# Kernel optimization log

Hardware: AMD Instinct MI355X
Metric: run time of the kernel (lower is better)

The kernel has to match this reference:

```python
import jax, jax.numpy as jnp
import numpy as np

LATENT = 256
HIDDEN = 512
NODE_F = 128
MAX_NODES = 50
B = 128


def _mk_linear(key, fan_in, fan_out):
    kw, kb = jax.random.split(key)
    bound = 1.0 / np.sqrt(fan_in)
    W = jax.random.uniform(kw, (fan_in, fan_out), jnp.float32, -bound, bound)
    b = jax.random.uniform(kb, (fan_out,), jnp.float32, -bound, bound)
    return W, b


def setup_inputs() -> dict:
    key = jax.random.key(0)
    ks = jax.random.split(key, 7)
    z = jax.random.normal(ks[0], (B, LATENT), jnp.float32)
    # node decoder: latent -> hidden -> hidden -> max_nodes*node_features
    nw1, nb1 = _mk_linear(ks[1], LATENT, HIDDEN)
    nw2, nb2 = _mk_linear(ks[2], HIDDEN, HIDDEN)
    nw3, nb3 = _mk_linear(ks[3], HIDDEN, MAX_NODES * NODE_F)
    # edge decoder: latent + 2*node_features -> hidden -> hidden//2 -> 1
    ew1, eb1 = _mk_linear(ks[4], LATENT + 2 * NODE_F, HIDDEN)
    ew2, eb2 = _mk_linear(ks[5], HIDDEN, HIDDEN // 2)
    ew3, eb3 = _mk_linear(ks[6], HIDDEN // 2, 1)
    return {"z": z,
            "nw1": nw1, "nb1": nb1, "nw2": nw2, "nb2": nb2, "nw3": nw3, "nb3": nb3,
            "ew1": ew1, "eb1": eb1, "ew2": ew2, "eb2": eb2, "ew3": ew3, "eb3": eb3}


def reference(z, nw1, nb1, nw2, nb2, nw3, nb3, ew1, eb1, ew2, eb2, ew3, eb3):
    # ---- node decoder ----
    h = jax.nn.relu(z @ nw1 + nb1)
    h = jax.nn.relu(h @ nw2 + nb2)
    node_logits = h @ nw3 + nb3                      # [B, MAX_NODES*NODE_F]
    node_feats = node_logits.reshape(z.shape[0], MAX_NODES, NODE_F)
    node_probs = jax.nn.sigmoid(node_feats)

    # ---- edge decoder: vectorize the O(N^2) python loop over upper-tri pairs ----
    # jnp.triu_indices matches the torch loop order: i ascending, j ascending per i.
    ii, jj = jnp.triu_indices(MAX_NODES, k=1)        # [P] each, P = 1225
    ni = node_feats[:, ii, :]                        # [B, P, NODE_F]
    nj = node_feats[:, jj, :]                        # [B, P, NODE_F]
    zb = jnp.broadcast_to(z[:, None, :], (z.shape[0], ii.shape[0], z.shape[1]))
    edge_in = jnp.concatenate([zb, ni, nj], axis=-1)  # [B, P, LATENT+2*NODE_F]
    e = jax.nn.relu(edge_in @ ew1 + eb1)             # [B, P, HIDDEN]
    e = jax.nn.relu(e @ ew2 + eb2)                   # [B, P, HIDDEN//2]
    edge_probs = jax.nn.sigmoid(e @ ew3 + eb3)[..., 0]  # [B, P]
    return node_probs, edge_probs
```

## Files before the change

kernel.cpp:

```cpp
#include <hip/hip_runtime.h>
#include <math.h>

#define LATENT 256
#define HIDDEN 512
#define NODE_F 128
#define MAX_NODES 50
#define NPAIRS 1225
#define BATCH 128
#define NODE_OUT 6400
#define MTILE 64
#define PTILES 20

typedef __attribute__((ext_vector_type(8))) short short8;
typedef __attribute__((ext_vector_type(4))) float float4v;

__device__ __forceinline__ float bf2f(ushort u) {
    union { unsigned int i; float f; } v; v.i = ((unsigned int)u) << 16; return v.f;
}
__device__ __forceinline__ ushort f2bf(float f) {
    union { unsigned int i; float f; } v; v.f = f;
    unsigned int r = v.i + 0x7fffu + ((v.i >> 16) & 1u);
    return (ushort)(r >> 16);
}
__device__ __forceinline__ float sigmoidf(float x) {
    return 1.0f / (1.0f + __expf(-x));
}

#define TR3_B0   0
#define PREP_B0  800
#define ZC_B0    1824
#define ND_B0    2080
#define PT_B0    2336
#define PREPK_NB 2341

__global__ __launch_bounds__(256) void k_prep_all(
    const float* __restrict__ nw3, ushort* __restrict__ nw3T,
    const float* __restrict__ ew1, const float* __restrict__ ew2,
    ushort* __restrict__ ew2T, ushort* __restrict__ wijT,
    const float* __restrict__ z, const float* __restrict__ eb1,
    float* __restrict__ Zc,
    const float* __restrict__ nw1, const float* __restrict__ nb1,
    const float* __restrict__ nw2, const float* __restrict__ nb2,
    ushort* __restrict__ h2b, int* __restrict__ ptab)
{
    __shared__ float smem[64 * 65];
    int b = blockIdx.x;
    int tid = threadIdx.x;

    if (b < PREP_B0) {
        int bb = b - TR3_B0;
        int k0 = (bb & 7) * 64;
        int n0 = (bb >> 3) * 64;
        int tx = tid & 63, ty = tid >> 6;
#pragma unroll
        for (int r = 0; r < 16; r++) {
            int row = r * 4 + ty;
            smem[row * 65 + tx] = nw3[(k0 + row) * NODE_OUT + n0 + tx];
        }
        __syncthreads();
#pragma unroll
        for (int c = 0; c < 16; c++) {
            int n = c * 4 + ty;
            nw3T[(size_t)(n0 + n) * HIDDEN + k0 + tx] = f2bf(smem[tx * 65 + n]);
        }
    } else if (b < ZC_B0) {
        int t = (b - PREP_B0) * 256 + tid;
        if (t < 256 * 512) {
            int n = t >> 9, k = t & 511;
            ew2T[t] = f2bf(ew2[k * 256 + n]);
        } else {
            int u = t - 256 * 512;
            int n = u >> 7, k = u & 127;
            float s = (n < 512) ? ew1[(256 + k) * 512 + n] : ew1[(384 + k) * 512 + (n - 512)];
            wijT[u] = f2bf(s);
        }
    } else if (b < ND_B0) {
        int b2 = b - ZC_B0;
        int r = b2 >> 1, o = (b2 & 1) * 256 + tid;
        float* zs = smem;
        zs[tid] = z[r * LATENT + tid];
        __syncthreads();
        float acc = 0.f;
#pragma unroll 8
        for (int k = 0; k < LATENT; k++) acc += zs[k] * ew1[k * HIDDEN + o];
        Zc[r * HIDDEN + o] = acc + eb1[o];
    } else if (b < PT_B0) {
        int b2 = b - ND_B0;
        int r = b2 >> 1, half = b2 & 1;
        float* zs = smem;
        float* hs = smem + 256;
        zs[tid] = z[r * LATENT + tid];
        __syncthreads();
        float a0 = 0.f, a1 = 0.f;
#pragma unroll 8
        for (int k = 0; k < LATENT; k++) {
            float zk = zs[k];
            a0 += zk * nw1[k * HIDDEN + tid];
            a1 += zk * nw1[k * HIDDEN + tid + 256];
        }
        hs[tid]       = fmaxf(a0 + nb1[tid], 0.f);
        hs[tid + 256] = fmaxf(a1 + nb1[tid + 256], 0.f);
        __syncthreads();
        int o = half * 256 + tid;
        float acc = 0.f;
#pragma unroll 8
        for (int k = 0; k < HIDDEN; k++) acc += hs[k] * nw2[k * HIDDEN + o];
        acc += nb2[o];
        h2b[r * HIDDEN + o] = f2bf(fmaxf(acc, 0.f));
    } else {
        int p = (b - PT_B0) * 256 + tid;
        if (p < NPAIRS) {
            int i = 0, off = 0;
            while (p - off >= MAX_NODES - 1 - i) { off += MAX_NODES - 1 - i; ++i; }
            int j = i + 1 + (p - off);
            ptab[p] = (i << 8) | j;
        }
    }
}

__global__ __launch_bounds__(256, 4) void k_node_out_mfma(
    const ushort* __restrict__ h2b, const ushort* __restrict__ nw3T,
    const float* __restrict__ nb3, float* __restrict__ node_probs,
    ushort* __restrict__ node_feats)
{
    int tid = threadIdx.x;
    int wave = tid >> 6, lane = tid & 63;
    int m16 = lane & 15, quad = lane >> 4;
    int n0 = (blockIdx.x >> 2) * 64;
    int m0 = (blockIdx.x & 3) * 32;
    int col = n0 + wave * 16 + m16;

    float4v acc[2];
    acc[0] = (float4v)(0.f); acc[1] = (float4v)(0.f);

    const ushort* bb = nw3T + (size_t)col * HIDDEN;
    const ushort* a0p = h2b + (m0 + m16) * HIDDEN;
    const ushort* a1p = h2b + (m0 + 16 + m16) * HIDDEN;
#pragma unroll
    for (int it = 0; it < 16; ++it) {
        int kk = it * 32 + quad * 8;
        short8 b = *(const short8*)(bb + kk);
        short8 a0 = *(const short8*)(a0p + kk);
        short8 a1 = *(const short8*)(a1p + kk);
        acc[0] = __builtin_amdgcn_mfma_f32_16x16x32_bf16(a0, b, acc[0], 0, 0, 0);
        acc[1] = __builtin_amdgcn_mfma_f32_16x16x32_bf16(a1, b, acc[1], 0, 0, 0);
    }
    float bias = nb3[col];
#pragma unroll
    for (int mt = 0; mt < 2; mt++)
#pragma unroll
        for (int t = 0; t < 4; t++) {
            int row = m0 + mt * 16 + quad * 4 + t;
            float v = acc[mt][t] + bias;
            node_probs[(size_t)row * NODE_OUT + col] = sigmoidf(v);
            node_feats[(size_t)row * NODE_OUT + col] = f2bf(v);
        }
}

__global__ __launch_bounds__(256, 4) void k_uv(
    const ushort* __restrict__ nf, const ushort* __restrict__ wijT,
    ushort* __restrict__ UV)
{
    int tid = threadIdx.x;
    int wave = tid >> 6, lane = tid & 63;
    int m16 = lane & 15, quad = lane >> 4;
    int bm = blockIdx.x >> 2, bn = blockIdx.x & 3;
    int base = bn * 256 + wave * 64;
    int r0 = bm * 64;

    float4v acc[4][4];
#pragma unroll
    for (int mt = 0; mt < 4; mt++)
#pragma unroll
        for (int nt = 0; nt < 4; nt++) acc[mt][nt] = (float4v)(0.f);

#pragma unroll
    for (int k0 = 0; k0 < NODE_F; k0 += 32) {
        int kk = k0 + quad * 8;
        short8 a0 = *(const short8*)(nf + (r0 + m16) * NODE_F + kk);
        short8 a1 = *(const short8*)(nf + (r0 + 16 + m16) * NODE_F + kk);
        short8 a2 = *(const short8*)(nf + (r0 + 32 + m16) * NODE_F + kk);
        short8 a3 = *(const short8*)(nf + (r0 + 48 + m16) * NODE_F + kk);
#pragma unroll
        for (int nt = 0; nt < 4; nt++) {
            int n = base + nt * 16 + m16;
            short8 b = *(const short8*)(wijT + n * NODE_F + kk);
            acc[0][nt] = __builtin_amdgcn_mfma_f32_16x16x32_bf16(a0, b, acc[0][nt], 0, 0, 0);
            acc[1][nt] = __builtin_amdgcn_mfma_f32_16x16x32_bf16(a1, b, acc[1][nt], 0, 0, 0);
            acc[2][nt] = __builtin_amdgcn_mfma_f32_16x16x32_bf16(a2, b, acc[2][nt], 0, 0, 0);
            acc[3][nt] = __builtin_amdgcn_mfma_f32_16x16x32_bf16(a3, b, acc[3][nt], 0, 0, 0);
        }
    }
#pragma unroll
    for (int nt = 0; nt < 4; nt++) {
        int colg = base + nt * 16 + m16;
#pragma unroll
        for (int mt = 0; mt < 4; mt++)
#pragma unroll
            for (int t = 0; t < 4; t++) {
                int rr = r0 + mt * 16 + quad * 4 + t;
                UV[(size_t)rr * 1024 + colg] = f2bf(acc[mt][nt][t]);
            }
    }
}

__global__ __launch_bounds__(512, 4) void k_edge6(
    const float* __restrict__ Zc, const ushort* __restrict__ UV,
    const ushort* __restrict__ ew2T, const float* __restrict__ ew3,
    const float* __restrict__ eb2, const float* __restrict__ eb3,
    const int* __restrict__ ptab, float* __restrict__ out_edges)
{
    __shared__ __align__(16) ushort h1[MTILE][HIDDEN + 8];
    __shared__ float part[MTILE][8];
    __shared__ int uo[MTILE], vo[MTILE];

    int blk = blockIdx.x;
    int b   = blk / PTILES;
    int t0  = (blk - b * PTILES) * MTILE;

    int tid = threadIdx.x;
    if (tid < MTILE) {
        int p = t0 + tid;
        if (p >= NPAIRS) p = NPAIRS - 1;
        int ij = ptab[p];
        uo[tid] = (b * MAX_NODES + (ij >> 8)) * 1024;
        vo[tid] = (b * MAX_NODES + (ij & 255)) * 1024 + 512;
    }

    int wave = tid >> 6, lane = tid & 63;
    int c8 = lane * 8;
    float4v zA = *(const float4v*)(Zc + b * HIDDEN + c8);
    float4v zB = *(const float4v*)(Zc + b * HIDDEN + c8 + 4);
    __syncthreads();

    short8 uu[8], vv[8];
#pragma unroll
    for (int rr = 0; rr < 8; rr++) {
        int r = wave * 8 + rr;
        uu[rr] = *(const short8*)(UV + uo[r] + c8);
        vv[rr] = *(const short8*)(UV + vo[r] + c8);
    }
#pragma unroll
    for (int rr = 0; rr < 8; rr++) {
        int r = wave * 8 + rr;
        short8 hh;
#pragma unroll
        for (int e = 0; e < 8; e++) {
            float zz = (e < 4) ? zA[e] : zB[e - 4];
            hh[e] = (short)f2bf(fmaxf(zz + bf2f((ushort)uu[rr][e]) + bf2f((ushort)vv[rr][e]), 0.f));
        }
        *(short8*)&h1[r][c8] = hh;
    }
    __syncthreads();

    int m16 = lane & 15, quad = lane >> 4;

    float eb2v[2], ew3v[2];
    const ushort* bbase[2];
#pragma unroll
    for (int nt = 0; nt < 2; nt++) {
        int col = wave * 32 + nt * 16 + m16;
        eb2v[nt] = eb2[col];
        ew3v[nt] = ew3[col];
        bbase[nt] = ew2T + col * HIDDEN;
    }

    float4v acc2[4][2];
#pragma unroll
    for (int mt = 0; mt < 4; mt++)
#pragma unroll
        for (int nt = 0; nt < 2; nt++) acc2[mt][nt] = (float4v)(0.f);

    int kk0 = quad * 8;
    short8 bp[2][2][2];
#pragma unroll
    for (int i = 0; i < 2; i++) {
        bp[0][i][0] = *(const short8*)(bbase[0] + i * 32 + kk0);
        bp[0][i][1] = *(const short8*)(bbase[1] + i * 32 + kk0);
    }
#pragma unroll
    for (int g = 0; g < 8; g++) {
        int cur = g & 1, nxt = cur ^ 1;
        if (g < 7) {
#pragma unroll
            for (int i = 0; i < 2; i++) {
                int kk = (g + 1) * 64 + i * 32 + kk0;
                bp[nxt][i][0] = *(const short8*)(bbase[0] + kk);
                bp[nxt][i][1] = *(const short8*)(bbase[1] + kk);
            }
        }
#pragma unroll
        for (int i = 0; i < 2; i++) {
            int kk = g * 64 + i * 32 + kk0;
            short8 a0 = *(const short8*)&h1[m16][kk];
            short8 a1 = *(const short8*)&h1[16 + m16][kk];
            short8 a2 = *(const short8*)&h1[32 + m16][kk];
            short8 a3 = *(const short8*)&h1[48 + m16][kk];
            acc2[0][0] = __builtin_amdgcn_mfma_f32_16x16x32_bf16(a0, bp[cur][i][0], acc2[0][0], 0, 0, 0);
            acc2[1][0] = __builtin_amdgcn_mfma_f32_16x16x32_bf16(a1, bp[cur][i][0], acc2[1][0], 0, 0, 0);
            acc2[2][0] = __builtin_amdgcn_mfma_f32_16x16x32_bf16(a2, bp[cur][i][0], acc2[2][0], 0, 0, 0);
            acc2[3][0] = __builtin_amdgcn_mfma_f32_16x16x32_bf16(a3, bp[cur][i][0], acc2[3][0], 0, 0, 0);
            acc2[0][1] = __builtin_amdgcn_mfma_f32_16x16x32_bf16(a0, bp[cur][i][1], acc2[0][1], 0, 0, 0);
            acc2[1][1] = __builtin_amdgcn_mfma_f32_16x16x32_bf16(a1, bp[cur][i][1], acc2[1][1], 0, 0, 0);
            acc2[2][1] = __builtin_amdgcn_mfma_f32_16x16x32_bf16(a2, bp[cur][i][1], acc2[2][1], 0, 0, 0);
            acc2[3][1] = __builtin_amdgcn_mfma_f32_16x16x32_bf16(a3, bp[cur][i][1], acc2[3][1], 0, 0, 0);
        }
    }

#pragma unroll
    for (int mt = 0; mt < 4; mt++)
#pragma unroll
        for (int t = 0; t < 4; t++) {
            float s = 0.f;
#pragma unroll
            for (int nt = 0; nt < 2; nt++)
                s += fmaxf(acc2[mt][nt][t] + eb2v[nt], 0.f) * ew3v[nt];
            s += __shfl_xor(s, 1);
            s += __shfl_xor(s, 2);
            s += __shfl_xor(s, 4);
            s += __shfl_xor(s, 8);
            if (m16 == 0) part[mt * 16 + quad * 4 + t][wave] = s;
        }
    __syncthreads();

    if (tid < MTILE && t0 + tid < NPAIRS) {
        float v = eb3[0];
#pragma unroll
        for (int w = 0; w < 8; w++) v += part[tid][w];
        out_edges[b * NPAIRS + t0 + tid] = sigmoidf(v);
    }
}

extern "C" void kernel_launch(void* const* d_in, const int* in_sizes, int n_in,
                              void* d_out, int out_size, void* d_ws, size_t ws_size,
                              hipStream_t stream) {
    const float* z   = (const float*)d_in[0];
    const float* nw1 = (const float*)d_in[1];
    const float* nb1 = (const float*)d_in[2];
    const float* nw2 = (const float*)d_in[3];
    const float* nb2 = (const float*)d_in[4];
    const float* nw3 = (const float*)d_in[5];
    const float* nb3 = (const float*)d_in[6];
    const float* ew1 = (const float*)d_in[7];
    const float* eb1 = (const float*)d_in[8];
    const float* ew2 = (const float*)d_in[9];
    const float* eb2 = (const float*)d_in[10];
    const float* ew3 = (const float*)d_in[11];
    const float* eb3 = (const float*)d_in[12];

    char* ws = (char*)d_ws;
    int*    ptab = (int*)(ws);
    ushort* h2b  = (ushort*)(ws + 262144);
    ushort* nf   = (ushort*)(ws + 393216);
    ushort* ew2T = (ushort*)(ws + 2031616);
    ushort* wijT = (ushort*)(ws + 2293760);
    ushort* nw3T = (ushort*)(ws + 2555904);
    float*  Zc   = (float*)(ws + 9109504);
    ushort* UV   = (ushort*)(ws + 9371648);

    float* out_nodes = (float*)d_out;
    float* out_edges = out_nodes + BATCH * NODE_OUT;

    k_prep_all<<<PREPK_NB, 256, 0, stream>>>(nw3, nw3T, ew1, ew2, ew2T, wijT,
                                             z, eb1, Zc, nw1, nb1, nw2, nb2,
                                             h2b, ptab);
    k_node_out_mfma<<<400, 256, 0, stream>>>(h2b, nw3T, nb3, out_nodes, nf);
    k_uv<<<400, 256, 0, stream>>>(nf, wijT, UV);
    k_edge6<<<BATCH * PTILES, 512, 0, stream>>>(Zc, UV, ew2T, ew3,
                                                eb2, eb3, ptab, out_edges);
}
```

Measured before the change: 243.4 us.

## Make edge kernel persistent over five tiles with register-resident weights and double-buffered h1

The edge kernel now runs 512 blocks, each handling five 64-pair tiles for one batch element, instead of one block per tile. Each wave loads its ew2 slice into registers once and reuses it across all five tiles, removing the repeated global weight loads. The h1 buffer in shared memory is double-buffered, so the UV gather and relu for the next tile are interleaved with the MFMA loop of the current tile. The costs are heavy register use (launch bounds drop to 2 blocks per CU), twice the shared memory, and fewer total blocks, which may reduce occupancy and latency hiding.

Measured after the change: 232.4 us. 4.5% less time.

```diff
diff --git a/kernel.cpp b/kernel.cpp
--- a/kernel.cpp
+++ b/kernel.cpp
@@ -9,7 +9,8 @@
 #define BATCH 128
 #define NODE_OUT 6400
 #define MTILE 64
-#define PTILES 20
+#define TPB 5
+#define EDGE_BLOCKS 512
 
 typedef __attribute__((ext_vector_type(8))) short short8;
 typedef __attribute__((ext_vector_type(4))) float float4v;
@@ -204,130 +205,179 @@
     }
 }
 
-__global__ __launch_bounds__(512, 4) void k_edge6(
+__global__ __launch_bounds__(512, 2) void k_edge7(
     const float* __restrict__ Zc, const ushort* __restrict__ UV,
     const ushort* __restrict__ ew2T, const float* __restrict__ ew3,
     const float* __restrict__ eb2, const float* __restrict__ eb3,
     const int* __restrict__ ptab, float* __restrict__ out_edges)
 {
-    __shared__ __align__(16) ushort h1[MTILE][HIDDEN + 8];
+    __shared__ __align__(16) ushort h1[2][MTILE][HIDDEN + 8];
     __shared__ float part[MTILE][8];
-    __shared__ int uo[MTILE], vo[MTILE];
-
-    int blk = blockIdx.x;
-    int b   = blk / PTILES;
-    int t0  = (blk - b * PTILES) * MTILE;
-
-    int tid = threadIdx.x;
+    __shared__ int uo5[TPB][MTILE], vo5[TPB][MTILE];
+
+    int tid  = threadIdx.x;
+    int blk  = blockIdx.x;
+    int b    = blk >> 2;
+    int ti0  = (blk & 3) * TPB;
+
     if (tid < MTILE) {
-        int p = t0 + tid;
-        if (p >= NPAIRS) p = NPAIRS - 1;
-        int ij = ptab[p];
-        uo[tid] = (b * MAX_NODES + (ij >> 8)) * 1024;
-        vo[tid] = (b * MAX_NODES + (ij & 255)) * 1024 + 512;
+#pragma unroll
+        for (int t = 0; t < TPB; t++) {
+            int p = (ti0 + t) * MTILE + tid;
+            if (p >= NPAIRS) p = NPAIRS - 1;
+            int ij = ptab[p];
+            uo5[t][tid] = (b * MAX_NODES + (ij >> 8)) * 1024;
+            vo5[t][tid] = (b * MAX_NODES + (ij & 255)) * 1024 + 512;
+        }
     }
 
     int wave = tid >> 6, lane = tid & 63;
+    int m16 = lane & 15, quad = lane >> 4;
     int c8 = lane * 8;
+    int kk0 = quad * 8;
+
     float4v zA = *(const float4v*)(Zc + b * HIDDEN + c8);
     float4v zB = *(const float4v*)(Zc + b * HIDDEN + c8 + 4);
+
+    const ushort* bb0 = ew2T + (wave * 32 + m16) * HIDDEN;
+    const ushort* bb1 = ew2T + (wave * 32 + 16 + m16) * HIDDEN;
+    short8 Breg[16][2];
+#pragma unroll
+    for (int kc = 0; kc < 16; kc++) {
+        Breg[kc][0] = *(const short8*)(bb0 + kc * 32 + kk0);
+        Breg[kc][1] = *(const short8*)(bb1 + kc * 32 + kk0);
+    }
+    float eb2v[2], ew3v[2];
+    eb2v[0] = eb2[wave * 32 + m16];      eb2v[1] = eb2[wave * 32 + 16 + m16];
+    ew3v[0] = ew3[wave * 32 + m16];      ew3v[1] = ew3[wave * 32 + 16 + m16];
+
     __syncthreads();
 
-    short8 uu[8], vv[8];
 #pragma unroll
     for (int rr = 0; rr < 8; rr++) {
         int r = wave * 8 + rr;
-        uu[rr] = *(const short8*)(UV + uo[r] + c8);
-        vv[rr] = *(const short8*)(UV + vo[r] + c8);
-    }
-#pragma unroll
-    for (int rr = 0; rr < 8; rr++) {
-        int r = wave * 8 + rr;
+        short8 u8 = *(const short8*)(UV + uo5[0][r] + c8);
+        short8 v8 = *(const short8*)(UV + vo5[0][r] + c8);
         short8 hh;
 #pragma unroll
         for (int e = 0; e < 8; e++) {
             float zz = (e < 4) ? zA[e] : zB[e - 4];
-            hh[e] = (short)f2bf(fmaxf(zz + bf2f((ushort)uu[rr][e]) + bf2f((ushort)vv[rr][e]), 0.f));
-        }
-        *(short8*)&h1[r][c8] = hh;
+            hh[e] = (short)f2bf(fmaxf(zz + bf2f((ushort)u8[e]) + bf2f((ushort)v8[e]), 0.f));
+        }
+        *(short8*)&h1[0][r][c8] = hh;
     }
     __syncthreads();
 
-    int m16 = lane & 15, quad = lane >> 4;
-
-    float eb2v[2], ew3v[2];
-    const ushort* bbase[2];
-#pragma unroll
-    for (int nt = 0; nt < 2; nt++) {
-        int col = wave * 32 + nt * 16 + m16;
-        eb2v[nt] = eb2[col];
-        ew3v[nt] = ew3[col];
-        bbase[nt] = ew2T + col * HIDDEN;
-    }
-
-    float4v acc2[4][2];
-#pragma unroll
-    for (int mt = 0; mt < 4; mt++)
-#pragma unroll
-        for (int nt = 0; nt < 2; nt++) acc2[mt][nt] = (float4v)(0.f);
-
-    int kk0 = quad * 8;
-    short8 bp[2][2][2];
-#pragma unroll
-    for (int i = 0; i < 2; i++) {
-        bp[0][i][0] = *(const short8*)(bbase[0] + i * 32 + kk0);
-        bp[0][i][1] = *(const short8*)(bbase[1] + i * 32 + kk0);
-    }
-#pragma unroll
-    for (int g = 0; g < 8; g++) {
-        int cur = g & 1, nxt = cur ^ 1;
-        if (g < 7) {
-#pragma unroll
-            for (int i = 0; i < 2; i++) {
-                int kk = (g + 1) * 64 + i * 32 + kk0;
-                bp[nxt][i][0] = *(const short8*)(bbase[0] + kk);
-                bp[nxt][i][1] = *(const short8*)(bbase[1] + kk);
-            }
-        }
-#pragma unroll
-        for (int i = 0; i < 2; i++) {
-            int kk = g * 64 + i * 32 + kk0;
-            short8 a0 = *(const short8*)&h1[m16][kk];
-            short8 a1 = *(const short8*)&h1[16 + m16][kk];
-            short8 a2 = *(const short8*)&h1[32 + m16][kk];
-            short8 a3 = *(const short8*)&h1[48 + m16][kk];
-            acc2[0][0] = __builtin_amdgcn_mfma_f32_16x16x32_bf16(a0, bp[cur][i][0], acc2[0][0], 0, 0, 0);
-            acc2[1][0] = __builtin_amdgcn_mfma_f32_16x16x32_bf16(a1, bp[cur][i][0], acc2[1][0], 0, 0, 0);
-            acc2[2][0] = __builtin_amdgcn_mfma_f32_16x16x32_bf16(a2, bp[cur][i][0], acc2[2][0], 0, 0, 0);
-            acc2[3][0] = __builtin_amdgcn_mfma_f32_16x16x32_bf16(a3, bp[cur][i][0], acc2[3][0], 0, 0, 0);
-            acc2[0][1] = __builtin_amdgcn_mfma_f32_16x16x32_bf16(a0, bp[cur][i][1], acc2[0][1], 0, 0, 0);
-            acc2[1][1] = __builtin_amdgcn_mfma_f32_16x16x32_bf16(a1, bp[cur][i][1], acc2[1][1], 0, 0, 0);
-            acc2[2][1] = __builtin_amdgcn_mfma_f32_16x16x32_bf16(a2, bp[cur][i][1], acc2[2][1], 0, 0, 0);
-            acc2[3][1] = __builtin_amdgcn_mfma_f32_16x16x32_bf16(a3, bp[cur][i][1], acc2[3][1], 0, 0, 0);
-        }
-    }
-
-#pragma unroll
-    for (int mt = 0; mt < 4; mt++)
-#pragma unroll
-        for (int t = 0; t < 4; t++) {
-            float s = 0.f;
-#pragma unroll
-            for (int nt = 0; nt < 2; nt++)
-                s += fmaxf(acc2[mt][nt][t] + eb2v[nt], 0.f) * ew3v[nt];
-            s += __shfl_xor(s, 1);
-            s += __shfl_xor(s, 2);
-            s += __shfl_xor(s, 4);
-            s += __shfl_xor(s, 8);
-            if (m16 == 0) part[mt * 16 + quad * 4 + t][wave] = s;
-        }
-    __syncthreads();
-
-    if (tid < MTILE && t0 + tid < NPAIRS) {
-        float v = eb3[0];
-#pragma unroll
-        for (int w = 0; w < 8; w++) v += part[tid][w];
-        out_edges[b * NPAIRS + t0 + tid] = sigmoidf(v);
+    for (int t = 0; t < TPB; t++) {
+        int cur = t & 1, nxt = cur ^ 1;
+        bool hasNext = (t + 1 < TPB);
+
+        float4v acc2[4][2];
+#pragma unroll
+        for (int mt = 0; mt < 4; mt++)
+#pragma unroll
+            for (int nt = 0; nt < 2; nt++) acc2[mt][nt] = (float4v)(0.f);
+
+        short8 uu[4], vv[4];
+        if (hasNext) {
+#pragma unroll
+            for (int rr = 0; rr < 4; rr++) {
+                int r = wave * 8 + rr;
+                uu[rr] = *(const short8*)(UV + uo5[t + 1][r] + c8);
+                vv[rr] = *(const short8*)(UV + vo5[t + 1][r] + c8);
+            }
+        }
+#pragma unroll
+        for (int it = 0; it < 8; ++it) {
+            int kk = it * 32 + kk0;
+            short8 a0 = *(const short8*)&h1[cur][m16][kk];
+            short8 a1 = *(const short8*)&h1[cur][16 + m16][kk];
+            short8 a2 = *(const short8*)&h1[cur][32 + m16][kk];
+            short8 a3 = *(const short8*)&h1[cur][48 + m16][kk];
+            acc2[0][0] = __builtin_amdgcn_mfma_f32_16x16x32_bf16(a0, Breg[it][0], acc2[0][0], 0, 0, 0);
+            acc2[1][0] = __builtin_amdgcn_mfma_f32_16x16x32_bf16(a1, Breg[it][0], acc2[1][0], 0, 0, 0);
+            acc2[2][0] = __builtin_amdgcn_mfma_f32_16x16x32_bf16(a2, Breg[it][0], acc2[2][0], 0, 0, 0);
+            acc2[3][0] = __builtin_amdgcn_mfma_f32_16x16x32_bf16(a3, Breg[it][0], acc2[3][0], 0, 0, 0);
+            acc2[0][1] = __builtin_amdgcn_mfma_f32_16x16x32_bf16(a0, Breg[it][1], acc2[0][1], 0, 0, 0);
+            acc2[1][1] = __builtin_amdgcn_mfma_f32_16x16x32_bf16(a1, Breg[it][1], acc2[1][1], 0, 0, 0);
+            acc2[2][1] = __builtin_amdgcn_mfma_f32_16x16x32_bf16(a2, Breg[it][1], acc2[2][1], 0, 0, 0);
+            acc2[3][1] = __builtin_amdgcn_mfma_f32_16x16x32_bf16(a3, Breg[it][1], acc2[3][1], 0, 0, 0);
+        }
+        if (hasNext) {
+#pragma unroll
+            for (int rr = 0; rr < 4; rr++) {
+                int r = wave * 8 + rr;
+                short8 hh;
+#pragma unroll
+                for (int e = 0; e < 8; e++) {
+                    float zz = (e < 4) ? zA[e] : zB[e - 4];
+                    hh[e] = (short)f2bf(fmaxf(zz + bf2f((ushort)uu[rr][e]) + bf2f((ushort)vv[rr][e]), 0.f));
+                }
+                *(short8*)&h1[nxt][r][c8] = hh;
+            }
+#pragma unroll
+            for (int rr = 0; rr < 4; rr++) {
+                int r = wave * 8 + 4 + rr;
+                uu[rr] = *(const short8*)(UV + uo5[t + 1][r] + c8);
+                vv[rr] = *(const short8*)(UV + vo5[t + 1][r] + c8);
+            }
+        }
+#pragma unroll
+        for (int it = 8; it < 16; ++it) {
+            int kk = it * 32 + kk0;
+            short8 a0 = *(const short8*)&h1[cur][m16][kk];
+            short8 a1 = *(const short8*)&h1[cur][16 + m16][kk];
+            short8 a2 = *(const short8*)&h1[cur][32 + m16][kk];
+            short8 a3 = *(const short8*)&h1[cur][48 + m16][kk];
+            acc2[0][0] = __builtin_amdgcn_mfma_f32_16x16x32_bf16(a0, Breg[it][0], acc2[0][0], 0, 0, 0);
+            acc2[1][0] = __builtin_amdgcn_mfma_f32_16x16x32_bf16(a1, Breg[it][0], acc2[1][0], 0, 0, 0);
+            acc2[2][0] = __builtin_amdgcn_mfma_f32_16x16x32_bf16(a2, Breg[it][0], acc2[2][0], 0, 0, 0);
+            acc2[3][0] = __builtin_amdgcn_mfma_f32_16x16x32_bf16(a3, Breg[it][0], acc2[3][0], 0, 0, 0);
+            acc2[0][1] = __builtin_amdgcn_mfma_f32_16x16x32_bf16(a0, Breg[it][1], acc2[0][1], 0, 0, 0);
+            acc2[1][1] = __builtin_amdgcn_mfma_f32_16x16x32_bf16(a1, Breg[it][1], acc2[1][1], 0, 0, 0);
+            acc2[2][1] = __builtin_amdgcn_mfma_f32_16x16x32_bf16(a2, Breg[it][1], acc2[2][1], 0, 0, 0);
+            acc2[3][1] = __builtin_amdgcn_mfma_f32_16x16x32_bf16(a3, Breg[it][1], acc2[3][1], 0, 0, 0);
+        }
+        if (hasNext) {
+#pragma unroll
+            for (int rr = 0; rr < 4; rr++) {
+                int r = wave * 8 + 4 + rr;
+                short8 hh;
+#pragma unroll
+                for (int e = 0; e < 8; e++) {
+                    float zz = (e < 4) ? zA[e] : zB[e - 4];
+                    hh[e] = (short)f2bf(fmaxf(zz + bf2f((ushort)uu[rr][e]) + bf2f((ushort)vv[rr][e]), 0.f));
+                }
+                *(short8*)&h1[nxt][r][c8] = hh;
+            }
+        }
+
+#pragma unroll
+        for (int mt = 0; mt < 4; mt++)
+#pragma unroll
+            for (int tt = 0; tt < 4; tt++) {
+                float s = 0.f;
+#pragma unroll
+                for (int nt = 0; nt < 2; nt++)
+                    s += fmaxf(acc2[mt][nt][tt] + eb2v[nt], 0.f) * ew3v[nt];
+                s += __shfl_xor(s, 1);
+                s += __shfl_xor(s, 2);
+                s += __shfl_xor(s, 4);
+                s += __shfl_xor(s, 8);
+                if (m16 == 0) part[mt * 16 + quad * 4 + tt][wave] = s;
+            }
+        __syncthreads();
+
+        if (tid < MTILE) {
+            int p = (ti0 + t) * MTILE + tid;
+            if (p < NPAIRS) {
+                float v = eb3[0];
+#pragma unroll
+                for (int w = 0; w < 8; w++) v += part[tid][w];
+                out_edges[b * NPAIRS + p] = sigmoidf(v);
+            }
+        }
+        __syncthreads();
     }
 }
 
@@ -366,6 +416,6 @@
                                              h2b, ptab);
     k_node_out_mfma<<<400, 256, 0, stream>>>(h2b, nw3T, nb3, out_nodes, nf);
     k_uv<<<400, 256, 0, stream>>>(nf, wijT, UV);
-    k_edge6<<<BATCH * PTILES, 512, 0, stream>>>(Zc, UV, ew2T, ew3,
-                                                eb2, eb3, ptab, out_edges);
-}
+    k_edge7<<<EDGE_BLOCKS, 512, 0, stream>>>(Zc, UV, ew2T, ew3,
+                                             eb2, eb3, ptab, out_edges);
+}
```
